# Performance work log

Measured on AMD Instinct MI355X. Metric: run time of the kernel, lower is better.

## Reference

```python
import jax, jax.numpy as jnp
import numpy as np

B, S, F = 4, 2048, 128
H, D = 4, 128          # num_heads, hidden_dim
OUT = 128              # out_features
NEG_SLOPE = 0.01       # torch leaky_relu default


def setup_inputs() -> dict:
    key = jax.random.key(0)
    ks = jax.random.split(key, 8)
    h = jax.random.normal(ks[0], (B, S, F), dtype=jnp.float32)
    # bool mask, True = masked-out key position (as used by masked_fill_)
    mask = jax.random.randint(ks[1], (B, S), 0, 2).astype(jnp.bool_)
    # Linear params (torch Linear: y = x @ W.T + b), kaiming-ish scale
    W_w = jax.random.normal(ks[2], (H * D, F), dtype=jnp.float32) / np.sqrt(F)
    W_b = jnp.zeros((H * D,), dtype=jnp.float32)
    a_w = jax.random.normal(ks[3], (1, 2 * D), dtype=jnp.float32) / np.sqrt(2 * D)
    a_b = jnp.zeros((1,), dtype=jnp.float32)
    out_w = jax.random.normal(ks[4], (OUT, H * D), dtype=jnp.float32) / np.sqrt(H * D)
    out_b = jnp.zeros((OUT,), dtype=jnp.float32)
    return {"h": h, "mask": mask, "W_w": W_w, "W_b": W_b,
            "a_w": a_w, "a_b": a_b, "out_w": out_w, "out_b": out_b}


def reference(h, mask, W_w, W_b, a_w, a_b, out_w, out_b):
    # h: [B,S,F] -> per-head projection hp: [B,H,S,D]
    hp = (h @ W_w.T + W_b).reshape(B, S, H, D).transpose(0, 2, 1, 3)
    # Additive GAT score a([h_i, h_j]) splits into two rank-1 contributions:
    # score[b,n,i,j] = leaky_relu(a1 . h_i + a2 . h_j + b)  (same math as the
    # original full [B,H,S,S,2D] concat + Linear, without materializing it).
    a1, a2 = a_w[0, :D], a_w[0, D:]
    e1 = jnp.einsum('bhsd,d->bhs', hp, a1)  # query-side term
    e2 = jnp.einsum('bhsd,d->bhs', hp, a2)  # key-side term
    scores = jax.nn.leaky_relu(e1[..., :, None] + e2[..., None, :] + a_b[0],
                               negative_slope=NEG_SLOPE)  # [B,H,S,S]
    # mask broadcast to [B,1,1,S]: masks key positions
    scores = jnp.where(mask[:, None, None, :], -jnp.inf, scores)
    attn = jax.nn.softmax(scores, axis=-1)  # [B,H,S,S]
    ctx = jnp.einsum('bhij,bhjd->bhid', attn, hp)  # [B,H,S,D]
    ctx = ctx.transpose(0, 2, 1, 3).reshape(B, S, H * D)
    out = jax.nn.relu(ctx @ out_w.T + out_b)  # [B,S,OUT]
    return out, attn
```

## Files before the change

kernel.cpp:

```cpp
#include <hip/hip_runtime.h>
#include <hip/hip_bf16.h>

#define BB 4
#define SS 2048
#define FF 128
#define DD 128
#define HD 512
#define OUTD 128
#define BH 16
#define NSL 0.01f
#define NC 258
#define NCH 32
#define CHK 64

typedef __hip_bfloat16 bf16;
typedef short bf16x8 __attribute__((ext_vector_type(8)));
typedef float f32x4 __attribute__((ext_vector_type(4)));

constexpr size_t OFF_HPF  = 0;
constexpr size_t OFF_E1   = OFF_HPF + (size_t)BB*SS*HD;
constexpr size_t OFF_M2   = OFF_E1 + (size_t)BH*SS;
constexpr size_t OFF_U    = OFF_M2 + 64;
constexpr size_t OFF_V    = OFF_U + (size_t)BH*SS;
constexpr size_t OFF_SIG  = OFF_V + (size_t)BH*SS;
constexpr size_t OFF_RARR = OFF_SIG + (size_t)BH*SS;
constexpr size_t OFF_WV   = OFF_RARR + (size_t)BH*SS;
constexpr size_t OFF_PL   = OFF_WV + 1024;
constexpr size_t OFF_CS   = OFF_PL + (size_t)BH*2049*NC;
constexpr size_t OFF_O    = OFF_CS + (size_t)BH*NCH*NC;
constexpr size_t OFF_TOT  = OFF_O + (size_t)BH*NCH*NC;
constexpr size_t OFF_CTX  = OFF_TOT + (size_t)BH*NC;

__device__ inline void load8_split(const float* __restrict__ p, bf16x8& hi, bf16x8& lo) {
  f32x4 x0 = *(const f32x4*)p;
  f32x4 x1 = *(const f32x4*)(p + 4);
#pragma unroll
  for (int e = 0; e < 8; ++e) {
    float x = (e < 4) ? x0[e] : x1[e - 4];
    __hip_bfloat16 hb = __float2bfloat16(x);
    float hf = __bfloat162float(hb);
    __hip_bfloat16 lb = __float2bfloat16(x - hf);
    hi[e] = (short)__bfloat16_as_ushort(hb);
    lo[e] = (short)__bfloat16_as_ushort(lb);
  }
}

__global__ __launch_bounds__(128) void k0_wvec(const float* __restrict__ Ww, const float* __restrict__ aw,
                                               float* __restrict__ wv) {
  int which = blockIdx.x >> 2, hh = blockIdx.x & 3;
  int f = threadIdx.x;
  float acc = 0.f;
#pragma unroll 4
  for (int d = 0; d < DD; ++d)
    acc += Ww[(size_t)(hh*DD + d)*FF + f] * aw[which*DD + d];
  wv[which*512 + hh*DD + f] = acc;
}

__global__ __launch_bounds__(256) void k1_hp(const float* __restrict__ h, const float* __restrict__ Ww,
                                             const float* __restrict__ Wb, float* __restrict__ hpf) {
  int wid = threadIdx.x >> 6, lane = threadIdx.x & 63;
  int tile = blockIdx.x * 4 + wid;
  int mt = tile >> 5, nt = tile & 31;
  int s0 = mt * 16, n0 = nt * 16;
  int row = lane & 15, g = lane >> 4;
  const float* pa = h  + (size_t)(s0 + row) * FF + g * 8;
  const float* pb = Ww + (size_t)(n0 + row) * FF + g * 8;
  f32x4 acc = {0.f,0.f,0.f,0.f};
#pragma unroll
  for (int ks = 0; ks < 4; ++ks) {
    bf16x8 ah, al, bh_, bl;
    load8_split(pa + ks*32, ah, al);
    load8_split(pb + ks*32, bh_, bl);
    acc = __builtin_amdgcn_mfma_f32_16x16x32_bf16(ah, bh_, acc, 0, 0, 0);
    acc = __builtin_amdgcn_mfma_f32_16x16x32_bf16(ah, bl,  acc, 0, 0, 0);
    acc = __builtin_amdgcn_mfma_f32_16x16x32_bf16(al, bh_, acc, 0, 0, 0);
  }
  int col = lane & 15;
  float bias = Wb[n0 + col];
#pragma unroll
  for (int r = 0; r < 4; ++r) {
    int orow = g*4 + r;
    hpf[(size_t)(s0 + orow) * HD + n0 + col] = acc[r] + bias;
  }
}

__global__ __launch_bounds__(1024) void k2bc(const float* __restrict__ h, const int* __restrict__ mask,
                                             const float* __restrict__ wv, const float* __restrict__ abp,
                                             float* __restrict__ e1g, float* __restrict__ m2out,
                                             float* __restrict__ u, float* __restrict__ v,
                                             int* __restrict__ sig, int* __restrict__ rarr) {
  int bh = blockIdx.x; int b = bh >> 2, hh = bh & 3;
  int tid = threadIdx.x;
  int wvid = tid >> 6, lane = tid & 63;
  __shared__ float red[1024];
  __shared__ float e1s[SS];
  __shared__ float va[SS];
  __shared__ int ia[SS];
  float w1a = wv[hh*DD + lane],       w1b = wv[hh*DD + lane + 64];
  float w2a = wv[512 + hh*DD + lane], w2b = wv[512 + hh*DD + lane + 64];
  const float* hbase = h + (size_t)b*SS*FF;
  for (int s = wvid; s < SS; s += 16) {
    float xa = hbase[(size_t)s*FF + lane];
    float xb = hbase[(size_t)s*FF + lane + 64];
    float r1 = xa*w1a + xb*w1b;
    float r2 = xa*w2a + xb*w2b;
    for (int o = 32; o; o >>= 1) { r1 += __shfl_down(r1, o); r2 += __shfl_down(r2, o); }
    if (lane == 0) { e1s[s] = r1; va[s] = r2; ia[s] = s; }
  }
  __syncthreads();
  float mx = -1e30f;
  for (int j = tid; j < SS; j += 1024)
    if (!mask[b*SS + j]) mx = fmaxf(mx, va[j]);
  red[tid] = mx; __syncthreads();
  for (int st = 512; st; st >>= 1) {
    if (tid < st) red[tid] = fmaxf(red[tid], red[tid + st]);
    __syncthreads();
  }
  float m2 = red[0];
  if (tid == 0) m2out[bh] = m2;
  for (int j = tid; j < SS; j += 1024) {
    float d = va[j] - m2;
    int mk = mask[b*SS + j];
    u[(size_t)bh*SS + j] = mk ? 0.f : expf(d);
    v[(size_t)bh*SS + j] = mk ? 0.f : expf(NSL * d);
    e1g[(size_t)bh*SS + j] = e1s[j];
  }
  __syncthreads();
  for (int k = 2; k <= SS; k <<= 1) {
    for (int jj = k >> 1; jj > 0; jj >>= 1) {
      for (int p = tid; p < SS; p += 1024) {
        int l = p ^ jj;
        if (l > p) {
          bool up = ((p & k) == 0);
          float vp = va[p], vl = va[l];
          if ((vp > vl) == up) {
            va[p] = vl; va[l] = vp;
            int t = ia[p]; ia[p] = ia[l]; ia[l] = t;
          }
        }
      }
      __syncthreads();
    }
  }
  float ab = abp[0];
  for (int i = tid; i < SS; i += 1024) {
    sig[(size_t)bh*SS + i] = ia[i];
    float key = -e1s[i] - ab;
    int lo = 0, hi = SS;
    while (lo < hi) { int mid = (lo + hi) >> 1; if (va[mid] < key) lo = mid + 1; else hi = mid; }
    rarr[(size_t)bh*SS + i] = lo;
  }
}

__global__ __launch_bounds__(320) void k3a_prefix(const float* __restrict__ hpf, const float* __restrict__ u,
                                                  const float* __restrict__ v, const int* __restrict__ sig,
                                                  float* __restrict__ PL, float* __restrict__ CS) {
  int bh = blockIdx.x >> 5;
  int ch = blockIdx.x & (NCH - 1);
  int c = threadIdx.x;
  int b = bh >> 2, hh = bh & 3;
  __shared__ int   js[CHK];
  __shared__ float us[CHK], vs[CHK];
  if (c < CHK) {
    int j = sig[(size_t)bh*SS + ch*CHK + c];
    js[c] = j;
    us[c] = u[(size_t)bh*SS + j];
    vs[c] = v[(size_t)bh*SS + j];
  }
  __syncthreads();
  if (c >= NC) return;
  if (ch == 0) PL[((size_t)bh*2049 + 0)*NC + c] = 0.f;
  const float* hb = hpf + (size_t)b*SS*HD + hh*DD;
  float acc = 0.f;
  size_t plbase = ((size_t)bh*2049 + ch*CHK + 1)*NC + c;
#pragma unroll 8
  for (int r = 0; r < CHK; ++r) {
    float term;
    if (c < 128)      term = us[r] * hb[(size_t)js[r]*HD + c];
    else if (c < 256) term = vs[r] * hb[(size_t)js[r]*HD + (c-128)];
    else if (c == 256) term = us[r];
    else              term = vs[r];
    acc += term;
    PL[plbase + (size_t)r*NC] = acc;
  }
  CS[((size_t)bh*NCH + ch)*NC + c] = acc;
}

__global__ __launch_bounds__(320) void k3b_scan(const float* __restrict__ CS, float* __restrict__ O,
                                                float* __restrict__ Tot) {
  int bh = blockIdx.x; int c = threadIdx.x;
  if (c >= NC) return;
  float acc = 0.f;
  for (int ch = 0; ch < NCH; ++ch) {
    O[((size_t)bh*NCH + ch)*NC + c] = acc;
    acc += CS[((size_t)bh*NCH + ch)*NC + c];
  }
  Tot[(size_t)bh*NC + c] = acc;
}

__global__ __launch_bounds__(256) void k4_main(const float* __restrict__ e1, const float* __restrict__ m2arr,
                                               const float* __restrict__ u, const float* __restrict__ v,
                                               const float* __restrict__ PL, const float* __restrict__ O,
                                               const float* __restrict__ Tot,
                                               const float* __restrict__ abp,
                                               const int* __restrict__ rarr,
                                               float* __restrict__ ctx, float* __restrict__ attn) {
  int bh = blockIdx.x >> 6;
  int ib = blockIdx.x & 63;
  int b = bh >> 2, hh = bh & 3;
  __shared__ float u_s[SS];
  __shared__ float v_s[SS];
  __shared__ float tot_s[NC];
  for (int j = threadIdx.x; j < SS; j += 256) {
    u_s[j] = u[(size_t)bh*SS + j];
    v_s[j] = v[(size_t)bh*SS + j];
  }
  for (int c0 = threadIdx.x; c0 < NC; c0 += 256) tot_s[c0] = Tot[(size_t)bh*NC + c0];
  __syncthreads();
  int wid = threadIdx.x >> 6, lane = threadIdx.x & 63;
  float m2 = m2arr[bh];
  float ab = abp[0];
  float SuT = tot_s[256];
  for (int rr = wid; rr < 32; rr += 4) {
    int i = ib*32 + rr;
    int r = rarr[(size_t)bh*SS + i];
    float t = e1[(size_t)bh*SS + i] + ab + m2;
    float rm = t > 0.f ? t : NSL*t;
    float alpha = expf(t - rm);
    float beta  = expf(NSL*t - rm);
    float tau = -t;
    int ch = (r == 0) ? 0 : ((r - 1) >> 6);
    const float* PLrow = PL + ((size_t)bh*2049 + r)*NC;
    const float* Orow  = O  + ((size_t)bh*NCH + ch)*NC;
    float SU = PLrow[256] + Orow[256];
    float SV = PLrow[257] + Orow[257];
    float denom = alpha * (SuT - SU) + beta * SV;
    float inv = 1.f / denom;
    float ad = alpha * inv, bd = beta * inv;
#pragma unroll
    for (int d0 = 0; d0 < 2; ++d0) {
      int d = lane + 64*d0;
      float fu = PLrow[d]       + Orow[d];
      float fv = PLrow[128 + d] + Orow[128 + d];
      float cv = (alpha * (tot_s[d] - fu) + beta * fv) * inv;
      ctx[(size_t)(b*SS + i)*HD + hh*DD + d] = cv;
    }
    float utau = expf(tau);
    float* orow = attn + ((size_t)bh*SS + i)*SS;
#pragma unroll 2
    for (int it = 0; it < 8; ++it) {
      int j0 = it*256 + lane*4;
      f32x4 uu = *(const f32x4*)&u_s[j0];
      f32x4 vv = *(const f32x4*)&v_s[j0];
      f32x4 av;
#pragma unroll
      for (int e = 0; e < 4; ++e) av[e] = (uu[e] >= utau) ? ad*uu[e] : bd*vv[e];
      __builtin_nontemporal_store(av, (f32x4*)(orow + j0));
    }
  }
}

__global__ __launch_bounds__(256) void k5_out(const float* __restrict__ ctx, const float* __restrict__ W2,
                                              const float* __restrict__ b2, float* __restrict__ outp) {
  int wid = threadIdx.x >> 6, lane = threadIdx.x & 63;
  int s0 = blockIdx.x * 16;
  int n0 = wid * 32;
  int row = lane & 15, g = lane >> 4;
  const float* pa  = ctx + (size_t)(s0 + row) * HD + g * 8;
  const float* pb0 = W2  + (size_t)(n0 + row) * HD + g * 8;
  const float* pb1 = W2  + (size_t)(n0 + 16 + row) * HD + g * 8;
  f32x4 acc0 = {0.f,0.f,0.f,0.f}, acc1 = {0.f,0.f,0.f,0.f};
  for (int ks = 0; ks < 16; ++ks) {
    bf16x8 ah, al, b0h, b0l, b1h, b1l;
    load8_split(pa  + ks*32, ah,  al);
    load8_split(pb0 + ks*32, b0h, b0l);
    load8_split(pb1 + ks*32, b1h, b1l);
    acc0 = __builtin_amdgcn_mfma_f32_16x16x32_bf16(ah, b0h, acc0, 0,0,0);
    acc0 = __builtin_amdgcn_mfma_f32_16x16x32_bf16(ah, b0l, acc0, 0,0,0);
    acc0 = __builtin_amdgcn_mfma_f32_16x16x32_bf16(al, b0h, acc0, 0,0,0);
    acc1 = __builtin_amdgcn_mfma_f32_16x16x32_bf16(ah, b1h, acc1, 0,0,0);
    acc1 = __builtin_amdgcn_mfma_f32_16x16x32_bf16(ah, b1l, acc1, 0,0,0);
    acc1 = __builtin_amdgcn_mfma_f32_16x16x32_bf16(al, b1h, acc1, 0,0,0);
  }
  int col = lane & 15;
  float bias0 = b2[n0 + col];
  float bias1 = b2[n0 + 16 + col];
#pragma unroll
  for (int r2 = 0; r2 < 4; ++r2) {
    int orow = g*4 + r2;
    float v0 = acc0[r2] + bias0; v0 = v0 > 0.f ? v0 : 0.f;
    float v1 = acc1[r2] + bias1; v1 = v1 > 0.f ? v1 : 0.f;
    outp[(size_t)(s0 + orow)*OUTD + n0 + col]      = v0;
    outp[(size_t)(s0 + orow)*OUTD + n0 + 16 + col] = v1;
  }
}

extern "C" void kernel_launch(void* const* d_in, const int* in_sizes, int n_in,
                              void* d_out, int out_size, void* d_ws, size_t ws_size,
                              hipStream_t stream) {
  const float* h   = (const float*)d_in[0];
  const int* mask  = (const int*)d_in[1];
  const float* Ww  = (const float*)d_in[2];
  const float* Wb  = (const float*)d_in[3];
  const float* aw  = (const float*)d_in[4];
  const float* abp = (const float*)d_in[5];
  const float* W2  = (const float*)d_in[6];
  const float* b2  = (const float*)d_in[7];
  float* ws = (float*)d_ws;
  float* hpf = ws + OFF_HPF;
  float* e1  = ws + OFF_E1;
  float* m2  = ws + OFF_M2;
  float* u   = ws + OFF_U;
  float* v   = ws + OFF_V;
  int*   sig = (int*)(ws + OFF_SIG);
  int*   rarr= (int*)(ws + OFF_RARR);
  float* wv  = ws + OFF_WV;
  float* PL  = ws + OFF_PL;
  float* CS  = ws + OFF_CS;
  float* O   = ws + OFF_O;
  float* Tot = ws + OFF_TOT;
  float* ctx = ws + OFF_CTX;
  float* outp = (float*)d_out;
  float* attn = outp + (size_t)BB*SS*OUTD;

  k0_wvec<<<8, 128, 0, stream>>>(Ww, aw, wv);
  k1_hp<<<4096, 256, 0, stream>>>(h, Ww, Wb, hpf);
  k2bc<<<16, 1024, 0, stream>>>(h, mask, wv, abp, e1, m2, u, v, sig, rarr);
  k3a_prefix<<<BH*NCH, 320, 0, stream>>>(hpf, u, v, sig, PL, CS);
  k3b_scan<<<16, 320, 0, stream>>>(CS, O, Tot);
  k4_main<<<BH*64, 256, 0, stream>>>(e1, m2, u, v, PL, O, Tot, abp, rarr, ctx, attn);
  k5_out<<<512, 256, 0, stream>>>(ctx, W2, b2, outp);
}
```

Measured before the change: 521.9 us.

## Split score projection out, co-schedule hp GEMM with sort, fold chunk scan into main

Moves the e1/e2 projection into a separate widely parallel kernel, then launches one combined kernel in which 1024 blocks do the hp GEMM while 16 blocks do the per-head sort and masked exponent work. The 16 sort blocks no longer run alone on a nearly idle GPU. The chunk-offset scan kernel is removed: each k4 block recomputes the offsets from CS into shared memory. The attention store is switched from nontemporal to a normal store. The cost is one extra launch, the redundant per-block scan and e2 round-tripping through global memory. The 1024-thread GEMM blocks may also lower occupancy.

```diff
diff --git a/kernel.cpp b/kernel.cpp
--- a/kernel.cpp
+++ b/kernel.cpp
@@ -19,7 +19,8 @@
 
 constexpr size_t OFF_HPF  = 0;
 constexpr size_t OFF_E1   = OFF_HPF + (size_t)BB*SS*HD;
-constexpr size_t OFF_M2   = OFF_E1 + (size_t)BH*SS;
+constexpr size_t OFF_E2   = OFF_E1 + (size_t)BH*SS;
+constexpr size_t OFF_M2   = OFF_E2 + (size_t)BH*SS;
 constexpr size_t OFF_U    = OFF_M2 + 64;
 constexpr size_t OFF_V    = OFF_U + (size_t)BH*SS;
 constexpr size_t OFF_SIG  = OFF_V + (size_t)BH*SS;
@@ -27,9 +28,7 @@
 constexpr size_t OFF_WV   = OFF_RARR + (size_t)BH*SS;
 constexpr size_t OFF_PL   = OFF_WV + 1024;
 constexpr size_t OFF_CS   = OFF_PL + (size_t)BH*2049*NC;
-constexpr size_t OFF_O    = OFF_CS + (size_t)BH*NCH*NC;
-constexpr size_t OFF_TOT  = OFF_O + (size_t)BH*NCH*NC;
-constexpr size_t OFF_CTX  = OFF_TOT + (size_t)BH*NC;
+constexpr size_t OFF_CTX  = OFF_CS + (size_t)BH*NCH*NC;
 
 __device__ inline void load8_split(const float* __restrict__ p, bf16x8& hi, bf16x8& lo) {
   f32x4 x0 = *(const f32x4*)p;
@@ -56,57 +55,65 @@
   wv[which*512 + hh*DD + f] = acc;
 }
 
-__global__ __launch_bounds__(256) void k1_hp(const float* __restrict__ h, const float* __restrict__ Ww,
-                                             const float* __restrict__ Wb, float* __restrict__ hpf) {
+__global__ __launch_bounds__(256) void k2_e(const float* __restrict__ h, const float* __restrict__ wv,
+                                            float* __restrict__ e1g, float* __restrict__ e2g) {
   int wid = threadIdx.x >> 6, lane = threadIdx.x & 63;
-  int tile = blockIdx.x * 4 + wid;
-  int mt = tile >> 5, nt = tile & 31;
-  int s0 = mt * 16, n0 = nt * 16;
-  int row = lane & 15, g = lane >> 4;
-  const float* pa = h  + (size_t)(s0 + row) * FF + g * 8;
-  const float* pb = Ww + (size_t)(n0 + row) * FF + g * 8;
-  f32x4 acc = {0.f,0.f,0.f,0.f};
-#pragma unroll
-  for (int ks = 0; ks < 4; ++ks) {
-    bf16x8 ah, al, bh_, bl;
-    load8_split(pa + ks*32, ah, al);
-    load8_split(pb + ks*32, bh_, bl);
-    acc = __builtin_amdgcn_mfma_f32_16x16x32_bf16(ah, bh_, acc, 0, 0, 0);
-    acc = __builtin_amdgcn_mfma_f32_16x16x32_bf16(ah, bl,  acc, 0, 0, 0);
-    acc = __builtin_amdgcn_mfma_f32_16x16x32_bf16(al, bh_, acc, 0, 0, 0);
-  }
-  int col = lane & 15;
-  float bias = Wb[n0 + col];
-#pragma unroll
-  for (int r = 0; r < 4; ++r) {
-    int orow = g*4 + r;
-    hpf[(size_t)(s0 + orow) * HD + n0 + col] = acc[r] + bias;
-  }
-}
-
-__global__ __launch_bounds__(1024) void k2bc(const float* __restrict__ h, const int* __restrict__ mask,
-                                             const float* __restrict__ wv, const float* __restrict__ abp,
-                                             float* __restrict__ e1g, float* __restrict__ m2out,
-                                             float* __restrict__ u, float* __restrict__ v,
-                                             int* __restrict__ sig, int* __restrict__ rarr) {
-  int bh = blockIdx.x; int b = bh >> 2, hh = bh & 3;
+  int g = blockIdx.x * 4 + wid;
+  int b = g >> 11, s = g & 2047;
+  float xa = h[(size_t)g*FF + lane];
+  float xb = h[(size_t)g*FF + 64 + lane];
+#pragma unroll
+  for (int hh = 0; hh < 4; ++hh) {
+    float r1 = xa*wv[hh*DD + lane]       + xb*wv[hh*DD + 64 + lane];
+    float r2 = xa*wv[512 + hh*DD + lane] + xb*wv[512 + hh*DD + 64 + lane];
+    for (int o = 32; o; o >>= 1) { r1 += __shfl_down(r1, o); r2 += __shfl_down(r2, o); }
+    if (lane == 0) {
+      e1g[(size_t)(b*4 + hh)*SS + s] = r1;
+      e2g[(size_t)(b*4 + hh)*SS + s] = r2;
+    }
+  }
+}
+
+__global__ __launch_bounds__(1024) void kfused(const float* __restrict__ h, const float* __restrict__ Ww,
+                                               const float* __restrict__ Wb, float* __restrict__ hpf,
+                                               const float* __restrict__ e1g, const float* __restrict__ e2g,
+                                               const int* __restrict__ mask, const float* __restrict__ abp,
+                                               float* __restrict__ m2out, float* __restrict__ u,
+                                               float* __restrict__ v, int* __restrict__ sig,
+                                               int* __restrict__ rarr) {
+  __shared__ float red[1024];
+  __shared__ float va[SS];
+  __shared__ int   ia[SS];
   int tid = threadIdx.x;
-  int wvid = tid >> 6, lane = tid & 63;
-  __shared__ float red[1024];
-  __shared__ float e1s[SS];
-  __shared__ float va[SS];
-  __shared__ int ia[SS];
-  float w1a = wv[hh*DD + lane],       w1b = wv[hh*DD + lane + 64];
-  float w2a = wv[512 + hh*DD + lane], w2b = wv[512 + hh*DD + lane + 64];
-  const float* hbase = h + (size_t)b*SS*FF;
-  for (int s = wvid; s < SS; s += 16) {
-    float xa = hbase[(size_t)s*FF + lane];
-    float xb = hbase[(size_t)s*FF + lane + 64];
-    float r1 = xa*w1a + xb*w1b;
-    float r2 = xa*w2a + xb*w2b;
-    for (int o = 32; o; o >>= 1) { r1 += __shfl_down(r1, o); r2 += __shfl_down(r2, o); }
-    if (lane == 0) { e1s[s] = r1; va[s] = r2; ia[s] = s; }
-  }
+  if (blockIdx.x < 1024) {
+    int wid = tid >> 6, lane = tid & 63;
+    int tile = blockIdx.x * 16 + wid;
+    int mt = tile >> 5, nt = tile & 31;
+    int s0 = mt * 16, n0 = nt * 16;
+    int row = lane & 15, g = lane >> 4;
+    const float* pa = h  + (size_t)(s0 + row) * FF + g * 8;
+    const float* pb = Ww + (size_t)(n0 + row) * FF + g * 8;
+    f32x4 acc = {0.f,0.f,0.f,0.f};
+#pragma unroll
+    for (int ks = 0; ks < 4; ++ks) {
+      bf16x8 ah, al, bh_, bl;
+      load8_split(pa + ks*32, ah, al);
+      load8_split(pb + ks*32, bh_, bl);
+      acc = __builtin_amdgcn_mfma_f32_16x16x32_bf16(ah, bh_, acc, 0, 0, 0);
+      acc = __builtin_amdgcn_mfma_f32_16x16x32_bf16(ah, bl,  acc, 0, 0, 0);
+      acc = __builtin_amdgcn_mfma_f32_16x16x32_bf16(al, bh_, acc, 0, 0, 0);
+    }
+    int col = lane & 15;
+    float bias = Wb[n0 + col];
+#pragma unroll
+    for (int r = 0; r < 4; ++r) {
+      int orow = g*4 + r;
+      hpf[(size_t)(s0 + orow) * HD + n0 + col] = acc[r] + bias;
+    }
+    return;
+  }
+  int bh = blockIdx.x - 1024; int b = bh >> 2;
+  for (int j = tid; j < SS; j += 1024) { va[j] = e2g[(size_t)bh*SS + j]; ia[j] = j; }
   __syncthreads();
   float mx = -1e30f;
   for (int j = tid; j < SS; j += 1024)
@@ -123,7 +130,6 @@
     int mk = mask[b*SS + j];
     u[(size_t)bh*SS + j] = mk ? 0.f : expf(d);
     v[(size_t)bh*SS + j] = mk ? 0.f : expf(NSL * d);
-    e1g[(size_t)bh*SS + j] = e1s[j];
   }
   __syncthreads();
   for (int k = 2; k <= SS; k <<= 1) {
@@ -145,7 +151,7 @@
   float ab = abp[0];
   for (int i = tid; i < SS; i += 1024) {
     sig[(size_t)bh*SS + i] = ia[i];
-    float key = -e1s[i] - ab;
+    float key = -e1g[(size_t)bh*SS + i] - ab;
     int lo = 0, hi = SS;
     while (lo < hi) { int mid = (lo + hi) >> 1; if (va[mid] < key) lo = mid + 1; else hi = mid; }
     rarr[(size_t)bh*SS + i] = lo;
@@ -186,22 +192,9 @@
   CS[((size_t)bh*NCH + ch)*NC + c] = acc;
 }
 
-__global__ __launch_bounds__(320) void k3b_scan(const float* __restrict__ CS, float* __restrict__ O,
-                                                float* __restrict__ Tot) {
-  int bh = blockIdx.x; int c = threadIdx.x;
-  if (c >= NC) return;
-  float acc = 0.f;
-  for (int ch = 0; ch < NCH; ++ch) {
-    O[((size_t)bh*NCH + ch)*NC + c] = acc;
-    acc += CS[((size_t)bh*NCH + ch)*NC + c];
-  }
-  Tot[(size_t)bh*NC + c] = acc;
-}
-
 __global__ __launch_bounds__(256) void k4_main(const float* __restrict__ e1, const float* __restrict__ m2arr,
                                                const float* __restrict__ u, const float* __restrict__ v,
-                                               const float* __restrict__ PL, const float* __restrict__ O,
-                                               const float* __restrict__ Tot,
+                                               const float* __restrict__ PL, const float* __restrict__ CS,
                                                const float* __restrict__ abp,
                                                const int* __restrict__ rarr,
                                                float* __restrict__ ctx, float* __restrict__ attn) {
@@ -210,12 +203,21 @@
   int b = bh >> 2, hh = bh & 3;
   __shared__ float u_s[SS];
   __shared__ float v_s[SS];
+  __shared__ float O_s[NCH][NC];
   __shared__ float tot_s[NC];
   for (int j = threadIdx.x; j < SS; j += 256) {
     u_s[j] = u[(size_t)bh*SS + j];
     v_s[j] = v[(size_t)bh*SS + j];
   }
-  for (int c0 = threadIdx.x; c0 < NC; c0 += 256) tot_s[c0] = Tot[(size_t)bh*NC + c0];
+  for (int c0 = threadIdx.x; c0 < NC; c0 += 256) {
+    float acc = 0.f;
+#pragma unroll 8
+    for (int ch = 0; ch < NCH; ++ch) {
+      O_s[ch][c0] = acc;
+      acc += CS[((size_t)bh*NCH + ch)*NC + c0];
+    }
+    tot_s[c0] = acc;
+  }
   __syncthreads();
   int wid = threadIdx.x >> 6, lane = threadIdx.x & 63;
   float m2 = m2arr[bh];
@@ -231,7 +233,7 @@
     float tau = -t;
     int ch = (r == 0) ? 0 : ((r - 1) >> 6);
     const float* PLrow = PL + ((size_t)bh*2049 + r)*NC;
-    const float* Orow  = O  + ((size_t)bh*NCH + ch)*NC;
+    const float* Orow  = O_s[ch];
     float SU = PLrow[256] + Orow[256];
     float SV = PLrow[257] + Orow[257];
     float denom = alpha * (SuT - SU) + beta * SV;
@@ -255,7 +257,7 @@
       f32x4 av;
 #pragma unroll
       for (int e = 0; e < 4; ++e) av[e] = (uu[e] >= utau) ? ad*uu[e] : bd*vv[e];
-      __builtin_nontemporal_store(av, (f32x4*)(orow + j0));
+      *(f32x4*)(orow + j0) = av;
     }
   }
 }
@@ -309,6 +311,7 @@
   float* ws = (float*)d_ws;
   float* hpf = ws + OFF_HPF;
   float* e1  = ws + OFF_E1;
+  float* e2  = ws + OFF_E2;
   float* m2  = ws + OFF_M2;
   float* u   = ws + OFF_U;
   float* v   = ws + OFF_V;
@@ -317,17 +320,14 @@
   float* wv  = ws + OFF_WV;
   float* PL  = ws + OFF_PL;
   float* CS  = ws + OFF_CS;
-  float* O   = ws + OFF_O;
-  float* Tot = ws + OFF_TOT;
   float* ctx = ws + OFF_CTX;
   float* outp = (float*)d_out;
   float* attn = outp + (size_t)BB*SS*OUTD;
 
   k0_wvec<<<8, 128, 0, stream>>>(Ww, aw, wv);
-  k1_hp<<<4096, 256, 0, stream>>>(h, Ww, Wb, hpf);
-  k2bc<<<16, 1024, 0, stream>>>(h, mask, wv, abp, e1, m2, u, v, sig, rarr);
+  k2_e<<<2048, 256, 0, stream>>>(h, wv, e1, e2);
+  kfused<<<1040, 1024, 0, stream>>>(h, Ww, Wb, hpf, e1, e2, mask, abp, m2, u, v, sig, rarr);
   k3a_prefix<<<BH*NCH, 320, 0, stream>>>(hpf, u, v, sig, PL, CS);
-  k3b_scan<<<16, 320, 0, stream>>>(CS, O, Tot);
-  k4_main<<<BH*64, 256, 0, stream>>>(e1, m2, u, v, PL, O, Tot, abp, rarr, ctx, attn);
+  k4_main<<<BH*64, 256, 0, stream>>>(e1, m2, u, v, PL, CS, abp, rarr, ctx, attn);
   k5_out<<<512, 256, 0, stream>>>(ctx, W2, b2, outp);
 }
```

New measurement: 460.7 us. 1.13x faster.
